# Optimization experiments

Measured on AMD Instinct MI355X. Metric: run time of the kernel, lower is better.

Reference implementation:

```python
import jax, jax.numpy as jnp
import numpy as np

B, S, DIM = 2, 2048, 2048
H, KVH = 16, 8
HD = DIM // H            # 128
WIN = 512                # sliding window size
GLOB = 64                # global tokens
NEG = -1000000000.0


def _alibi_slopes(n):
    cp2 = 2.0 ** jnp.floor(jnp.log2(jnp.float32(n)))
    base = 2.0 ** (-(2.0 ** (-(jnp.log2(cp2) - 3.0))))
    powers = jnp.arange(1, 1 + n, dtype=jnp.float32)
    return jnp.power(base, powers)  # [n]


def _rope_tables(head_dim, seq_len, dtype=jnp.float32, base=10000.0):
    half = head_dim // 2
    freqs = 1.0 / base ** (jnp.arange(0, half, dtype=dtype) / half)
    t = jnp.arange(seq_len, dtype=dtype)
    f = jnp.outer(t, freqs)                       # [S, half]
    return jnp.sin(f)[None, None], jnp.cos(f)[None, None]  # [1,1,S,half]


def _rotary(x, sin, cos):
    # x: [b,h,s,d]; nonstandard rotation per source module
    x1, x2 = jnp.split(x, 2, axis=-1)
    return jnp.concatenate([x1 * cos - x2 * sin, x1 * sin + x2 * cos], axis=-1)


def _window_mask(seq_len):
    # Faithful to create_sliding_window_mask: 0.0 inside window / global rows+cols, -1e9 elsewhere
    i = jnp.arange(seq_len)[:, None]
    j = jnp.arange(seq_len)[None, :]
    m = jnp.where(jnp.abs(i - j) <= WIN // 2, 0.0, NEG)
    m = jnp.where((i < GLOB) | (j < GLOB), 0.0, m)
    return m  # [S, S] float


def setup_inputs() -> dict:
    key = jax.random.key(0)
    k1, k2, k3, k4 = jax.random.split(key, 4)
    x = jax.random.normal(k1, (B, S, DIM), dtype=jnp.float32)
    Wq = jax.random.normal(k2, (DIM, DIM), dtype=jnp.float32) * 0.02
    Wkv = jax.random.normal(k3, (DIM, 2 * KVH * HD), dtype=jnp.float32) * 0.02
    Wo = jax.random.normal(k4, (DIM, DIM), dtype=jnp.float32) * 0.02
    bo = jnp.zeros((DIM,), dtype=jnp.float32)
    return {"x": x, "Wq": Wq, "Wkv": Wkv, "Wo": Wo, "bo": bo}


def reference(x, Wq, Wkv, Wo, bo):
    b, s, dim = x.shape
    # token-complexity gating on queries
    complexity = jax.nn.sigmoid(jnp.sum(jnp.abs(x), axis=-1, keepdims=True))  # [b,s,1]
    q = jnp.dot(x * complexity, Wq)       # [b,s,dim]
    kv = jnp.dot(x, Wkv)                  # [b,s,2*kv_dim]
    k, v = jnp.split(kv, 2, axis=-1)

    q = q.reshape(b, s, H, HD).transpose(0, 2, 1, 3)      # [b,H,s,d]
    k = k.reshape(b, s, KVH, HD).transpose(0, 2, 1, 3)    # [b,KVH,s,d]
    v = v.reshape(b, s, KVH, HD).transpose(0, 2, 1, 3)

    sin, cos = _rope_tables(HD, s, dtype=x.dtype)
    q = _rotary(q, sin, cos)
    k = _rotary(k, sin, cos)

    r = H // KVH
    k = jnp.repeat(k, r, axis=1)   # 'b h s d -> b (h r) s d'
    v = jnp.repeat(v, r, axis=1)

    scale = 1.0 / jnp.sqrt(jnp.float32(HD)).astype(x.dtype)
    qk = jnp.einsum('bhid,bhjd->bhij', q, k) * scale      # [b,H,s,s]

    # ALiBi bias
    slopes = _alibi_slopes(H)                             # [H]
    pos = jnp.arange(s)
    dist = -jnp.abs(pos[:, None] - pos[None, :]).astype(jnp.float32)  # [s,s]
    qk = qk + slopes[:, None, None] * dist                # broadcast over batch

    # Faithful to source: jnp.where(float_mask, qk, NEG) treats nonzero (-1e9,
    # i.e. OUTSIDE window) as True -> keeps qk; zero (inside window) -> NEG.
    m = _window_mask(s)
    qk = jnp.where(m != 0.0, qk, NEG)

    attn = jax.nn.softmax(qk, axis=-1)
    out = jnp.einsum('bhij,bhjd->bhid', attn, v)          # [b,H,s,d]
    out = out.transpose(0, 2, 1, 3).reshape(b, s, dim)
    out = jnp.dot(out, Wo) + bo
    return out
```

## Files before the change

kernel.cpp:

```cpp
#include <hip/hip_runtime.h>

#define DEVI static __device__ __forceinline__

typedef __attribute__((ext_vector_type(8))) short short8;
typedef __attribute__((ext_vector_type(4))) short short4v;
typedef __attribute__((ext_vector_type(4))) float f32x4;

DEVI float bf2f(short u) {
  union { unsigned u32; float f; } c;
  c.u32 = ((unsigned)(unsigned short)u) << 16;
  return c.f;
}
DEVI short f2bf(float f) {
  union { float f; unsigned u32; } c; c.f = f;
  unsigned x = c.u32;
  unsigned r = (x + 0x7FFFu + ((x >> 16) & 1u)) >> 16;
  return (short)(unsigned short)r;
}
DEVI float ex2(float x) {
  float r;
  asm("v_exp_f32 %0, %1" : "=v"(r) : "v"(x));
  return r;
}
DEVI unsigned cvtpk(float lo, float hi) {
  unsigned r;
  asm("v_cvt_pk_bf16_f32 %0, %1, %2" : "=v"(r) : "v"(lo), "v"(hi));
  return r;
}

DEVI void gload16(const void* g, void* l) {
  __builtin_amdgcn_global_load_lds(
      (__attribute__((address_space(1))) void*)(g),
      (__attribute__((address_space(3))) void*)(l), 16, 0, 0);
}

#define LOG2E 1.4426950408889634f
#define QSCALE 0.1275174470974102f

__global__ void prep_x_kernel(const float* __restrict__ x,
                              short* __restrict__ xq, short* __restrict__ xb) {
  int row = blockIdx.x, t = threadIdx.x;
  const float4* xr = (const float4*)(x + (size_t)row * 2048);
  float4 v0 = xr[t], v1 = xr[t + 256];
  float s = fabsf(v0.x) + fabsf(v0.y) + fabsf(v0.z) + fabsf(v0.w)
          + fabsf(v1.x) + fabsf(v1.y) + fabsf(v1.z) + fabsf(v1.w);
#pragma unroll
  for (int m = 1; m < 64; m <<= 1) s += __shfl_xor(s, m, 64);
  __shared__ float red[4];
  if ((t & 63) == 0) red[t >> 6] = s;
  __syncthreads();
  float tot = red[0] + red[1] + red[2] + red[3];
  float sc = 1.0f / (1.0f + expf(-tot));
  short4v q0, q1, b0, b1;
  q0[0] = f2bf(v0.x * sc); q0[1] = f2bf(v0.y * sc); q0[2] = f2bf(v0.z * sc); q0[3] = f2bf(v0.w * sc);
  q1[0] = f2bf(v1.x * sc); q1[1] = f2bf(v1.y * sc); q1[2] = f2bf(v1.z * sc); q1[3] = f2bf(v1.w * sc);
  b0[0] = f2bf(v0.x); b0[1] = f2bf(v0.y); b0[2] = f2bf(v0.z); b0[3] = f2bf(v0.w);
  b1[0] = f2bf(v1.x); b1[1] = f2bf(v1.y); b1[2] = f2bf(v1.z); b1[3] = f2bf(v1.w);
  size_t base = (size_t)row * 512;
  ((short4v*)xq)[base + t]       = q0;
  ((short4v*)xq)[base + t + 256] = q1;
  ((short4v*)xb)[base + t]       = b0;
  ((short4v*)xb)[base + t + 256] = b1;
}

__global__ void sincos_kernel(float* __restrict__ tsin, float* __restrict__ tcos) {
  int idx = blockIdx.x * 256 + threadIdx.x;
  int d = idx >> 11, s = idx & 2047;
  float freq = powf(10000.0f, -(float)d / 64.0f);
  float f = (float)s * freq;
  tsin[idx] = sinf(f);
  tcos[idx] = cosf(f);
}

__global__ void wtrans_kernel(const float* __restrict__ W0, const float* __restrict__ W1,
                              const float* __restrict__ W2,
                              short* __restrict__ T0, short* __restrict__ T1,
                              short* __restrict__ T2) {
  __shared__ __align__(16) short tile[64][68];
  const float* W = blockIdx.z == 0 ? W0 : (blockIdx.z == 1 ? W1 : W2);
  short* WT      = blockIdx.z == 0 ? T0 : (blockIdx.z == 1 ? T1 : T2);
  int n0 = blockIdx.x * 64, k0 = blockIdx.y * 64;
  int t = threadIdx.x;
  int tr = t >> 4, tc = t & 15;
#pragma unroll
  for (int p = 0; p < 4; ++p) {
    int r = p * 16 + tr;
    int c = tc * 4;
    float4 v = *(const float4*)&W[(size_t)(k0 + r) * 2048 + n0 + c];
    tile[c + 0][r] = f2bf(v.x);
    tile[c + 1][r] = f2bf(v.y);
    tile[c + 2][r] = f2bf(v.z);
    tile[c + 3][r] = f2bf(v.w);
  }
  __syncthreads();
#pragma unroll
  for (int p = 0; p < 4; ++p) {
    int n = p * 16 + tr;
    int c = tc * 4;
    *(short4v*)&WT[(size_t)(n0 + n) * 2048 + k0 + c] = *(const short4v*)&tile[n][c];
  }
}

template<int EPI>
__launch_bounds__(256, 4)
__global__ void gemm_kernel(const short* __restrict__ A, const short* __restrict__ BT,
                            void* __restrict__ Cout, short* __restrict__ aux,
                            const float* __restrict__ bias,
                            const float* __restrict__ tsin, const float* __restrict__ tcos,
                            int M, int N, int K) {
  __shared__ __align__(16) short As[128 * 64];
  __shared__ __align__(16) short Bs[128 * 64];
  const int tid = threadIdx.x;
  const int wid = tid >> 6, lane = tid & 63;
  const int nb = gridDim.x * gridDim.y;
  const int orig = blockIdx.y * gridDim.x + blockIdx.x;
  const int swz = (orig & 7) * (nb >> 3) + (orig >> 3);
  const int m0 = (swz / gridDim.x) * 128, n0 = (swz % gridDim.x) * 128;
  const int l15 = lane & 15, l4 = lane >> 4;
  const int sw7 = l15 & 7;
  f32x4 acc[2][8] = {};
  for (int k0 = 0; k0 < K; k0 += 64) {
#pragma unroll
    for (int p = 0; p < 4; ++p) {
      int cid = p * 256 + tid;
      int row = cid >> 3, ch = cid & 7;
      int cole = (ch ^ (row & 7)) * 8;
      gload16(A + (size_t)(m0 + row) * K + k0 + cole, &As[cid * 8]);
      gload16(BT + (size_t)(n0 + row) * K + k0 + cole, &Bs[cid * 8]);
    }
    __syncthreads();
#pragma unroll
    for (int kk = 0; kk < 2; ++kk) {
      const int cc = ((kk * 4 + l4) ^ sw7) * 8;
      short8 af0 = *(const short8*)&As[(wid * 32 + l15) * 64 + cc];
      short8 af1 = *(const short8*)&As[(wid * 32 + 16 + l15) * 64 + cc];
      short8 bf0 = *(const short8*)&Bs[(0 * 16 + l15) * 64 + cc];
      short8 bf1 = *(const short8*)&Bs[(1 * 16 + l15) * 64 + cc];
      short8 bf2 = *(const short8*)&Bs[(2 * 16 + l15) * 64 + cc];
      short8 bf3 = *(const short8*)&Bs[(3 * 16 + l15) * 64 + cc];
      acc[0][0] = __builtin_amdgcn_mfma_f32_16x16x32_bf16(af0, bf0, acc[0][0], 0, 0, 0);
      acc[1][0] = __builtin_amdgcn_mfma_f32_16x16x32_bf16(af1, bf0, acc[1][0], 0, 0, 0);
      acc[0][1] = __builtin_amdgcn_mfma_f32_16x16x32_bf16(af0, bf1, acc[0][1], 0, 0, 0);
      acc[1][1] = __builtin_amdgcn_mfma_f32_16x16x32_bf16(af1, bf1, acc[1][1], 0, 0, 0);
      acc[0][2] = __builtin_amdgcn_mfma_f32_16x16x32_bf16(af0, bf2, acc[0][2], 0, 0, 0);
      acc[1][2] = __builtin_amdgcn_mfma_f32_16x16x32_bf16(af1, bf2, acc[1][2], 0, 0, 0);
      acc[0][3] = __builtin_amdgcn_mfma_f32_16x16x32_bf16(af0, bf3, acc[0][3], 0, 0, 0);
      acc[1][3] = __builtin_amdgcn_mfma_f32_16x16x32_bf16(af1, bf3, acc[1][3], 0, 0, 0);
      bf0 = *(const short8*)&Bs[(4 * 16 + l15) * 64 + cc];
      bf1 = *(const short8*)&Bs[(5 * 16 + l15) * 64 + cc];
      bf2 = *(const short8*)&Bs[(6 * 16 + l15) * 64 + cc];
      bf3 = *(const short8*)&Bs[(7 * 16 + l15) * 64 + cc];
      acc[0][4] = __builtin_amdgcn_mfma_f32_16x16x32_bf16(af0, bf0, acc[0][4], 0, 0, 0);
      acc[1][4] = __builtin_amdgcn_mfma_f32_16x16x32_bf16(af1, bf0, acc[1][4], 0, 0, 0);
      acc[0][5] = __builtin_amdgcn_mfma_f32_16x16x32_bf16(af0, bf1, acc[0][5], 0, 0, 0);
      acc[1][5] = __builtin_amdgcn_mfma_f32_16x16x32_bf16(af1, bf1, acc[1][5], 0, 0, 0);
      acc[0][6] = __builtin_amdgcn_mfma_f32_16x16x32_bf16(af0, bf2, acc[0][6], 0, 0, 0);
      acc[1][6] = __builtin_amdgcn_mfma_f32_16x16x32_bf16(af1, bf2, acc[1][6], 0, 0, 0);
      acc[0][7] = __builtin_amdgcn_mfma_f32_16x16x32_bf16(af0, bf3, acc[0][7], 0, 0, 0);
      acc[1][7] = __builtin_amdgcn_mfma_f32_16x16x32_bf16(af1, bf3, acc[1][7], 0, 0, 0);
    }
    __syncthreads();
  }

  if (EPI == 0) {
#pragma unroll
    for (int mi = 0; mi < 2; ++mi) {
#pragma unroll
      for (int ni = 0; ni < 8; ++ni) {
        int col = n0 + ni * 16 + l15;
        float badd = bias[col];
#pragma unroll
        for (int r = 0; r < 4; ++r) {
          int row = m0 + wid * 32 + mi * 16 + l4 * 4 + r;
          ((float*)Cout)[(size_t)row * N + col] = acc[mi][ni][r] + badd;
        }
      }
    }
  } else if (EPI == 1) {
    const int h = n0 >> 7;
    const int b = m0 >> 11;
    const int sb = (m0 & 2047) + wid * 32;
    short* qr = (short*)Cout;
    const size_t obase = ((size_t)(b * 16 + h) * 2048 + sb) * 128;
#pragma unroll
    for (int mi = 0; mi < 2; ++mi) {
      int srel = sb + mi * 16 + l4 * 4;
#pragma unroll
      for (int ni = 0; ni < 4; ++ni) {
        int d = ni * 16 + l15;
        float4 sn = *(const float4*)&tsin[d * 2048 + srel];
        float4 cs = *(const float4*)&tcos[d * 2048 + srel];
#pragma unroll
        for (int r = 0; r < 4; ++r) {
          float x1 = acc[mi][ni][r], x2 = acc[mi][ni + 4][r];
          float snr = (&sn.x)[r], csr = (&cs.x)[r];
          size_t ro = obase + (size_t)(mi * 16 + l4 * 4 + r) * 128;
          qr[ro + d]      = f2bf((x1 * csr - x2 * snr) * QSCALE);
          qr[ro + d + 64] = f2bf((x1 * snr + x2 * csr) * QSCALE);
        }
      }
    }
  } else {
    const int b = m0 >> 11;
    const int sb = (m0 & 2047) + wid * 32;
    if (n0 < 1024) {
      const int kvh = n0 >> 7;
      short* kr = (short*)Cout;
      const size_t obase = ((size_t)(b * 8 + kvh) * 2048 + sb) * 128;
#pragma unroll
      for (int mi = 0; mi < 2; ++mi) {
        int srel = sb + mi * 16 + l4 * 4;
#pragma unroll
        for (int ni = 0; ni < 4; ++ni) {
          int d = ni * 16 + l15;
          float4 sn = *(const float4*)&tsin[d * 2048 + srel];
          float4 cs = *(const float4*)&tcos[d * 2048 + srel];
#pragma unroll
          for (int r = 0; r < 4; ++r) {
            float x1 = acc[mi][ni][r], x2 = acc[mi][ni + 4][r];
            float snr = (&sn.x)[r], csr = (&cs.x)[r];
            size_t ro = obase + (size_t)(mi * 16 + l4 * 4 + r) * 128;
            kr[ro + d]      = f2bf(x1 * csr - x2 * snr);
            kr[ro + d + 64] = f2bf(x1 * snr + x2 * csr);
          }
        }
      }
    } else {
      const int kvh = (n0 - 1024) >> 7;
      short* vt = aux;
      const size_t vb = (size_t)(b * 8 + kvh) * 128;
#pragma unroll
      for (int mi = 0; mi < 2; ++mi) {
        int srel = sb + mi * 16 + l4 * 4;
#pragma unroll
        for (int ni = 0; ni < 8; ++ni) {
          int d = ni * 16 + l15;
          uint2 w;
          w.x = cvtpk(acc[mi][ni][0], acc[mi][ni][1]);
          w.y = cvtpk(acc[mi][ni][2], acc[mi][ni][3]);
          *(uint2*)&vt[(vb + d) * 2048 + srel] = w;
        }
      }
    }
  }
}

__launch_bounds__(512, 4)
__global__ void attn_kernel(const short* __restrict__ qr, const short* __restrict__ kr,
                            const short* __restrict__ vt, short* __restrict__ ob) {
  __shared__ __align__(16) short Ks[2][64 * 128];
  __shared__ __align__(16) short Vs[2][128 * 64];
  __shared__ __align__(16) short PL[8][16 * 64];
  const int tid = threadIdx.x;
  const int wid = tid >> 6, lane = tid & 63;
  const int l15 = lane & 15, l4 = lane >> 4;
  const int sw7 = l15 & 7;
  const int l4h = l4 >> 1, l4l = l4 & 1;
  const int f = blockIdx.x + (blockIdx.y << 4) + (blockIdx.z << 8);
  const int swb = (f & 7) * 64 + (f >> 3);
  const int qt = swb & 15, h = (swb >> 4) & 15, b = swb >> 8;
  const int kh = h >> 1;
  const int qb = qt * 128;
  const int q0 = qb + wid * 16;
  const float slope2 = exp2f(-0.5f * (float)(h + 1)) * LOG2E;
  const size_t qbase = ((size_t)(b * 16 + h) * 2048 + q0) * 128;
  const size_t kbase = ((size_t)(b * 8 + kh) * 2048) * 128;
  const size_t vbase = ((size_t)(b * 8 + kh) * 128) * 2048;
  short* pl = PL[wid];

  short8 aq[4];
#pragma unroll
  for (int kk = 0; kk < 4; ++kk)
    aq[kk] = *(const short8*)&qr[qbase + (size_t)l15 * 128 + kk * 32 + l4 * 8];

  f32x4 o[8] = {};
  float m_run = -1e30f, l_run = 0.0f;
  const int iq = q0 + l15;

  int lo0, n0t, lo1, n1t;
  if (qt == 0)      { lo0 = 0;   n0t = 32;          lo1 = 0; n1t = 0; }
  else if (qt == 1) { lo0 = 384; n0t = 26;          lo1 = 0; n1t = 0; }
  else {
    lo0 = 64;        n0t = 2 * qt - 3;
    lo1 = qb + 256;  n1t = (28 - 2 * qt > 0) ? (28 - 2 * qt) : 0;
  }
  const int nt = n0t + n1t;
  auto KV0 = [&](int i) { return i < n0t ? lo0 + i * 64 : lo1 + (i - n0t) * 64; };

  auto STAGE = [&](int bi, int kv0) {
#pragma unroll
    for (int i2 = 0; i2 < 2; ++i2) {
      int cid = i2 * 512 + tid;
      int krow = cid >> 4, kch = cid & 15;
      gload16(kr + kbase + (size_t)(kv0 + krow) * 128 + ((kch ^ (krow & 7)) * 8),
              &Ks[bi][cid * 8]);
    }
#pragma unroll
    for (int i2 = 0; i2 < 2; ++i2) {
      int cid = i2 * 512 + tid;
      int vrow = cid >> 3, vch = cid & 7;
      gload16(vt + vbase + (size_t)vrow * 2048 + kv0 + ((vch ^ (vrow & 7)) * 8),
              &Vs[bi][cid * 8]);
    }
  };

  STAGE(0, KV0(0));
  __syncthreads();
  int cur = 0;

  for (int it = 0; it < nt; ++it) {
    const int kv0 = KV0(it);
    if (it + 1 < nt) STAGE(cur ^ 1, KV0(it + 1));

    int mode;
    if (q0 + 15 < 64 || kv0 == 0) mode = 3;
    else if (kv0 <= q0 - 320)     mode = 1;
    else if (kv0 >= q0 + 272)     mode = 2;
    else                          mode = 0;

    if (mode != 3) {
      f32x4 sc[4];
#pragma unroll
      for (int jj = 0; jj < 4; ++jj) sc[jj] = (f32x4){0.f, 0.f, 0.f, 0.f};
      __builtin_amdgcn_s_setprio(1);
#pragma unroll
      for (int kk = 0; kk < 4; ++kk) {
#pragma unroll
        for (int jj = 0; jj < 4; ++jj) {
          short8 bk = *(const short8*)&Ks[cur][(jj * 16 + l15) * 128 + (((kk * 4 + l4) ^ sw7) * 8)];
          sc[jj] = __builtin_amdgcn_mfma_f32_16x16x32_bf16(bk, aq[kk], sc[jj], 0, 0, 0);
        }
      }
      __builtin_amdgcn_s_setprio(0);
      float pm = -1e30f;
      const float dbase = (float)(iq - kv0 - l4 * 4);
      if (mode == 0) {
#pragma unroll
        for (int jj = 0; jj < 4; ++jj) {
          float dj = dbase - 16.0f * jj;
#pragma unroll
          for (int r = 0; r < 4; ++r) {
            float d = dj - (float)r;
            float ad = fabsf(d);
            float v = fmaf(-slope2, ad, sc[jj][r]);
            v = (ad > 256.0f) ? v : -1e9f;
            sc[jj][r] = v;
            pm = fmaxf(pm, v);
          }
        }
      } else {
        const float sl = (mode == 1) ? -slope2 : slope2;
#pragma unroll
        for (int jj = 0; jj < 4; ++jj) {
          float dj = dbase - 16.0f * jj;
#pragma unroll
          for (int r = 0; r < 4; ++r) {
            float v = fmaf(sl, dj - (float)r, sc[jj][r]);
            sc[jj][r] = v;
            pm = fmaxf(pm, v);
          }
        }
      }
      pm = fmaxf(pm, __shfl_xor(pm, 16, 64));
      pm = fmaxf(pm, __shfl_xor(pm, 32, 64));
      if (!__all(pm <= m_run + 8.0f)) {
        float mn = fmaxf(m_run, pm);
        float corr = ex2(m_run - mn);
        l_run *= corr;
#pragma unroll
        for (int dn = 0; dn < 8; ++dn)
#pragma unroll
          for (int r = 0; r < 4; ++r) o[dn][r] *= corr;
        m_run = mn;
      }
      float psum = 0.0f;
#pragma unroll
      for (int jj = 0; jj < 4; ++jj) {
        float p0 = ex2(sc[jj][0] - m_run);
        float p1 = ex2(sc[jj][1] - m_run);
        float p2 = ex2(sc[jj][2] - m_run);
        float p3 = ex2(sc[jj][3] - m_run);
        psum += (p0 + p1) + (p2 + p3);
        uint2 w; w.x = cvtpk(p0, p1); w.y = cvtpk(p2, p3);
        int ad = l15 * 64 + (((jj * 2 + l4h) ^ sw7) * 8) + l4l * 4;
        *(uint2*)&pl[ad] = w;
      }
      psum += __shfl_xor(psum, 16, 64);
      psum += __shfl_xor(psum, 32, 64);
      l_run += psum;
      asm volatile("s_waitcnt lgkmcnt(0)" ::: "memory");
      __builtin_amdgcn_sched_barrier(0);
      __builtin_amdgcn_s_setprio(1);
#pragma unroll
      for (int c = 0; c < 2; ++c) {
        short8 pa = *(const short8*)&pl[l15 * 64 + (((c * 4 + l4) ^ sw7) * 8)];
#pragma unroll
        for (int dn = 0; dn < 8; ++dn) {
          short8 bv = *(const short8*)&Vs[cur][(dn * 16 + l15) * 64 + (((c * 4 + l4) ^ sw7) * 8)];
          o[dn] = __builtin_amdgcn_mfma_f32_16x16x32_bf16(bv, pa, o[dn], 0, 0, 0);
        }
      }
      __builtin_amdgcn_s_setprio(0);
    } else {
      float pm = -1e9f;
      if (!__all(pm <= m_run + 8.0f)) {
        float mn = fmaxf(m_run, pm);
        float corr = ex2(m_run - mn);
        l_run *= corr;
#pragma unroll
        for (int dn = 0; dn < 8; ++dn)
#pragma unroll
          for (int r = 0; r < 4; ++r) o[dn][r] *= corr;
        m_run = mn;
      }
      float pu = ex2(-1e9f - m_run);
      l_run += 64.0f * pu;
      unsigned uu = cvtpk(pu, pu);
      short8 pa;
      ((unsigned*)&pa)[0] = uu; ((unsigned*)&pa)[1] = uu;
      ((unsigned*)&pa)[2] = uu; ((unsigned*)&pa)[3] = uu;
      __builtin_amdgcn_s_setprio(1);
#pragma unroll
      for (int c = 0; c < 2; ++c) {
#pragma unroll
        for (int dn = 0; dn < 8; ++dn) {
          short8 bv = *(const short8*)&Vs[cur][(dn * 16 + l15) * 64 + (((c * 4 + l4) ^ sw7) * 8)];
          o[dn] = __builtin_amdgcn_mfma_f32_16x16x32_bf16(bv, pa, o[dn], 0, 0, 0);
        }
      }
      __builtin_amdgcn_s_setprio(0);
    }
    __syncthreads();
    cur ^= 1;
  }

  float inv = 1.0f / l_run;
  size_t rbase = ((size_t)(b * 2048 + iq) * 16 + h) * 128;
#pragma unroll
  for (int dn = 0; dn < 8; ++dn) {
    uint2 w;
    w.x = cvtpk(o[dn][0] * inv, o[dn][1] * inv);
    w.y = cvtpk(o[dn][2] * inv, o[dn][3] * inv);
    *(uint2*)&ob[rbase + dn * 16 + l4 * 4] = w;
  }
}

extern "C" void kernel_launch(void* const* d_in, const int* in_sizes, int n_in,
                              void* d_out, int out_size, void* d_ws, size_t ws_size,
                              hipStream_t stream) {
  const float* x   = (const float*)d_in[0];
  const float* Wq  = (const float*)d_in[1];
  const float* Wkv = (const float*)d_in[2];
  const float* Wo  = (const float*)d_in[3];
  const float* bo  = (const float*)d_in[4];
  float* out = (float*)d_out;

  char* ws = (char*)d_ws;
  size_t off = 0;
  auto alloc = [&](size_t bytes) -> void* {
    void* p = ws + off;
    off += (bytes + 255) & ~(size_t)255;
    return p;
  };
  float* tsin  = (float*)alloc(64 * 2048 * 4);
  float* tcos  = (float*)alloc(64 * 2048 * 4);
  short* WqT   = (short*)alloc((size_t)2048 * 2048 * 2);
  short* WkvT  = (short*)alloc((size_t)2048 * 2048 * 2);
  short* WoT   = (short*)alloc((size_t)2048 * 2048 * 2);
  short* xq    = (short*)alloc((size_t)4096 * 2048 * 2);
  short* xb    = (short*)alloc((size_t)4096 * 2048 * 2);
  short* qr    = (short*)alloc((size_t)2 * 16 * 2048 * 128 * 2);
  short* kr    = (short*)alloc((size_t)2 * 8 * 2048 * 128 * 2);
  short* vt    = (short*)alloc((size_t)2 * 8 * 2048 * 128 * 2);
  short* ob    = xq;

  prep_x_kernel<<<4096, 256, 0, stream>>>(x, xq, xb);
  sincos_kernel<<<512, 256, 0, stream>>>(tsin, tcos);
  wtrans_kernel<<<dim3(32, 32, 3), 256, 0, stream>>>(Wq, Wkv, Wo, WqT, WkvT, WoT);
  gemm_kernel<1><<<dim3(16, 32), 256, 0, stream>>>(xq, WqT, qr, nullptr, nullptr, tsin, tcos, 4096, 2048, 2048);
  gemm_kernel<2><<<dim3(16, 32), 256, 0, stream>>>(xb, WkvT, kr, vt, nullptr, tsin, tcos, 4096, 2048, 2048);
  attn_kernel<<<dim3(16, 16, 2), 512, 0, stream>>>(qr, kr, vt, ob);
  gemm_kernel<0><<<dim3(16, 32), 256, 0, stream>>>(ob, WoT, (void*)out, nullptr, bo, nullptr, nullptr, 4096, 2048, 2048);
  (void)in_sizes; (void)n_in; (void)out_size; (void)ws_size;
}
```

Measured before the change: 230.5 us.

## Double-buffer GEMM LDS tiles to overlap global loads with MFMA

Converts the GEMM main loop to a two-stage LDS pipeline: the next K-tile is issued with direct-to-LDS loads while the current tile is consumed, using an explicit vmcnt wait and raw barriers instead of __syncthreads. It also raises wave priority around MFMA bursts with s_setprio. LDS use doubles to 64KB per block and launch bounds drop to 2 blocks per CU, trading occupancy for latency hiding.

Measured after the change: 226.8 us. About the same (-1.6%).

```diff
diff --git a/kernel.cpp b/kernel.cpp
--- a/kernel.cpp
+++ b/kernel.cpp
@@ -102,14 +102,14 @@
 }
 
 template<int EPI>
-__launch_bounds__(256, 4)
+__launch_bounds__(256, 2)
 __global__ void gemm_kernel(const short* __restrict__ A, const short* __restrict__ BT,
                             void* __restrict__ Cout, short* __restrict__ aux,
                             const float* __restrict__ bias,
                             const float* __restrict__ tsin, const float* __restrict__ tcos,
                             int M, int N, int K) {
-  __shared__ __align__(16) short As[128 * 64];
-  __shared__ __align__(16) short Bs[128 * 64];
+  __shared__ __align__(16) short As[2][128 * 64];
+  __shared__ __align__(16) short Bs[2][128 * 64];
   const int tid = threadIdx.x;
   const int wid = tid >> 6, lane = tid & 63;
   const int nb = gridDim.x * gridDim.y;
@@ -118,26 +118,40 @@
   const int m0 = (swz / gridDim.x) * 128, n0 = (swz % gridDim.x) * 128;
   const int l15 = lane & 15, l4 = lane >> 4;
   const int sw7 = l15 & 7;
-  f32x4 acc[2][8] = {};
-  for (int k0 = 0; k0 < K; k0 += 64) {
+  const int T = K >> 6;
+
+  auto STAGE = [&](int bi, int t) {
 #pragma unroll
     for (int p = 0; p < 4; ++p) {
       int cid = p * 256 + tid;
       int row = cid >> 3, ch = cid & 7;
       int cole = (ch ^ (row & 7)) * 8;
-      gload16(A + (size_t)(m0 + row) * K + k0 + cole, &As[cid * 8]);
-      gload16(BT + (size_t)(n0 + row) * K + k0 + cole, &Bs[cid * 8]);
-    }
-    __syncthreads();
+      gload16(A + (size_t)(m0 + row) * K + t * 64 + cole, &As[bi][cid * 8]);
+      gload16(BT + (size_t)(n0 + row) * K + t * 64 + cole, &Bs[bi][cid * 8]);
+    }
+  };
+
+  f32x4 acc[2][8] = {};
+  STAGE(0, 0);
+  for (int t = 0; t < T; ++t) {
+    const int cur = t & 1;
+    if (t + 1 < T) {
+      STAGE(cur ^ 1, t + 1);
+      asm volatile("s_waitcnt vmcnt(8)" ::: "memory");
+    } else {
+      asm volatile("s_waitcnt vmcnt(0)" ::: "memory");
+    }
+    __builtin_amdgcn_s_barrier();
 #pragma unroll
     for (int kk = 0; kk < 2; ++kk) {
       const int cc = ((kk * 4 + l4) ^ sw7) * 8;
-      short8 af0 = *(const short8*)&As[(wid * 32 + l15) * 64 + cc];
-      short8 af1 = *(const short8*)&As[(wid * 32 + 16 + l15) * 64 + cc];
-      short8 bf0 = *(const short8*)&Bs[(0 * 16 + l15) * 64 + cc];
-      short8 bf1 = *(const short8*)&Bs[(1 * 16 + l15) * 64 + cc];
-      short8 bf2 = *(const short8*)&Bs[(2 * 16 + l15) * 64 + cc];
-      short8 bf3 = *(const short8*)&Bs[(3 * 16 + l15) * 64 + cc];
+      short8 af0 = *(const short8*)&As[cur][(wid * 32 + l15) * 64 + cc];
+      short8 af1 = *(const short8*)&As[cur][(wid * 32 + 16 + l15) * 64 + cc];
+      short8 bf0 = *(const short8*)&Bs[cur][(0 * 16 + l15) * 64 + cc];
+      short8 bf1 = *(const short8*)&Bs[cur][(1 * 16 + l15) * 64 + cc];
+      short8 bf2 = *(const short8*)&Bs[cur][(2 * 16 + l15) * 64 + cc];
+      short8 bf3 = *(const short8*)&Bs[cur][(3 * 16 + l15) * 64 + cc];
+      __builtin_amdgcn_s_setprio(1);
       acc[0][0] = __builtin_amdgcn_mfma_f32_16x16x32_bf16(af0, bf0, acc[0][0], 0, 0, 0);
       acc[1][0] = __builtin_amdgcn_mfma_f32_16x16x32_bf16(af1, bf0, acc[1][0], 0, 0, 0);
       acc[0][1] = __builtin_amdgcn_mfma_f32_16x16x32_bf16(af0, bf1, acc[0][1], 0, 0, 0);
@@ -146,10 +160,12 @@
       acc[1][2] = __builtin_amdgcn_mfma_f32_16x16x32_bf16(af1, bf2, acc[1][2], 0, 0, 0);
       acc[0][3] = __builtin_amdgcn_mfma_f32_16x16x32_bf16(af0, bf3, acc[0][3], 0, 0, 0);
       acc[1][3] = __builtin_amdgcn_mfma_f32_16x16x32_bf16(af1, bf3, acc[1][3], 0, 0, 0);
-      bf0 = *(const short8*)&Bs[(4 * 16 + l15) * 64 + cc];
-      bf1 = *(const short8*)&Bs[(5 * 16 + l15) * 64 + cc];
-      bf2 = *(const short8*)&Bs[(6 * 16 + l15) * 64 + cc];
-      bf3 = *(const short8*)&Bs[(7 * 16 + l15) * 64 + cc];
+      __builtin_amdgcn_s_setprio(0);
+      bf0 = *(const short8*)&Bs[cur][(4 * 16 + l15) * 64 + cc];
+      bf1 = *(const short8*)&Bs[cur][(5 * 16 + l15) * 64 + cc];
+      bf2 = *(const short8*)&Bs[cur][(6 * 16 + l15) * 64 + cc];
+      bf3 = *(const short8*)&Bs[cur][(7 * 16 + l15) * 64 + cc];
+      __builtin_amdgcn_s_setprio(1);
       acc[0][4] = __builtin_amdgcn_mfma_f32_16x16x32_bf16(af0, bf0, acc[0][4], 0, 0, 0);
       acc[1][4] = __builtin_amdgcn_mfma_f32_16x16x32_bf16(af1, bf0, acc[1][4], 0, 0, 0);
       acc[0][5] = __builtin_amdgcn_mfma_f32_16x16x32_bf16(af0, bf1, acc[0][5], 0, 0, 0);
@@ -158,8 +174,9 @@
       acc[1][6] = __builtin_amdgcn_mfma_f32_16x16x32_bf16(af1, bf2, acc[1][6], 0, 0, 0);
       acc[0][7] = __builtin_amdgcn_mfma_f32_16x16x32_bf16(af0, bf3, acc[0][7], 0, 0, 0);
       acc[1][7] = __builtin_amdgcn_mfma_f32_16x16x32_bf16(af1, bf3, acc[1][7], 0, 0, 0);
-    }
-    __syncthreads();
+      __builtin_amdgcn_s_setprio(0);
+    }
+    __builtin_amdgcn_s_barrier();
   }
 
   if (EPI == 0) {
```
